# Kernel optimization log

Hardware: AMD Instinct MI355X
Metric: run time of the kernel (lower is better)

## Reference

```python
import jax, jax.numpy as jnp
import numpy as np
from jax import lax

EPS = 1e-08


def setup_inputs() -> dict:
    key = jax.random.key(0)
    k1, k2, k3 = jax.random.split(key, 3)
    b, cin, cout, ks, h, w = 16, 64, 64, 3, 256, 256
    X = jax.random.normal(k1, (b, cin, h, w), dtype=jnp.float32)
    y = jax.random.normal(k2, (b, cin), dtype=jnp.float32)
    weight = jax.random.normal(k3, (cout, cin, ks, ks), dtype=jnp.float32)
    return {"X": X, "y": y, "weight": weight}


def reference(X, y, weight):
    # EqualizedWeight: scale by Kaiming constant c = (cin*k*k)^-0.5 (gain=lr_mul=1)
    cout, cin, ks, _ = weight.shape
    c = (cin * ks * ks) ** (-0.5)
    w0 = weight * c
    # Modulate: per-sample, per-input-channel scaling -> (b, cout, cin, k, k)
    w1 = w0[None] * y[:, None, :, None, None]
    # Demodulate: normalize each (sample, out-filter) to unit L2 norm
    d = lax.rsqrt(jnp.sum(w1 * w1, axis=(2, 3, 4), keepdims=True) + EPS)
    w1 = w1 * d
    b, _, h, w = X.shape
    # Grouped conv: fold batch into channels, one group per sample
    Xr = X.reshape(1, b * cin, h, w)
    ker = w1.reshape(b * cout, cin, ks, ks)
    out = lax.conv_general_dilated(
        Xr, ker,
        window_strides=(1, 1),
        padding="SAME",
        feature_group_count=b,
        dimension_numbers=("NCHW", "OIHW", "NCHW"),
    )
    return out.reshape(b, cout, h, w)
```

## Files before the change

kernel.cpp:

```cpp
#include <hip/hip_runtime.h>
#include <hip/hip_bf16.h>

typedef __bf16 bf16x8 __attribute__((ext_vector_type(8)));
typedef float  f32x4  __attribute__((ext_vector_type(4)));

#define B_   16
#define CIN  64
#define COUT 64
#define H_   256
#define W_   256
#define TY   16
#define SLOT (258 * 64)

__global__ void modw_kernel(const float* __restrict__ weight,
                            const float* __restrict__ y,
                            __bf16* __restrict__ w1g) {
  const int co = blockIdx.x;
  const int b  = blockIdx.y;
  const int ci = threadIdx.x;
  const float c  = 0.041666666666666664f;
  const float yv = y[b*CIN + ci] * c;
  float w[9];
  float s = 0.0f;
#pragma unroll
  for (int t = 0; t < 9; ++t) {
    float wv = weight[(co*CIN + ci)*9 + t] * yv;
    w[t] = wv;
    s += wv * wv;
  }
#pragma unroll
  for (int off = 32; off > 0; off >>= 1) s += __shfl_xor(s, off, 64);
  const float d = rsqrtf(s + 1e-8f);
#pragma unroll
  for (int t = 0; t < 9; ++t)
    w1g[((b*9 + t)*COUT + co)*CIN + ci] = (__bf16)(w[t] * d);
}

__device__ __forceinline__ void stage_load(const float* __restrict__ X,
                                           int b, int yy, int tid, float4* f) {
  const int cg = tid >> 6;
  const int px_base = 4 * (tid & 63);
  const float* xrow = X + ((long)b * (CIN * H_ * W_) + (long)yy * W_);
#pragma unroll
  for (int j = 0; j < 8; ++j)
    f[j] = *reinterpret_cast<const float4*>(xrow + (long)(cg * 8 + j) * (H_ * W_) + px_base);
}

__device__ __forceinline__ void stage_write(__bf16* __restrict__ xs, int slot,
                                            int tid, const float4* f, bool valid) {
  const int cg = tid >> 6;
  const int px_base = 4 * (tid & 63);
  bf16x8 frag[4];
  if (valid) {
#pragma unroll
    for (int j = 0; j < 8; ++j) {
      frag[0][j] = (__bf16)f[j].x;
      frag[1][j] = (__bf16)f[j].y;
      frag[2][j] = (__bf16)f[j].z;
      frag[3][j] = (__bf16)f[j].w;
    }
  } else {
#pragma unroll
    for (int o = 0; o < 4; ++o)
#pragma unroll
      for (int j = 0; j < 8; ++j) frag[o][j] = (__bf16)0.f;
  }
#pragma unroll
  for (int oo = 0; oo < 4; ++oo) {
    const int o  = (oo + tid) & 3;
    const int pl = px_base + o + 1;
    const int gs = cg ^ (pl & 7);
    *reinterpret_cast<bf16x8*>(&xs[slot * SLOT + pl * 64 + gs * 8]) = frag[o];
  }
}

__global__ __launch_bounds__(512, 2)
void conv_kernel(const float* __restrict__ X,
                 const __bf16* __restrict__ w1g,
                 float* __restrict__ out) {
  const int y0   = blockIdx.x * TY;
  const int b    = blockIdx.y;
  const int tid  = threadIdx.x;
  const int lane = tid & 63;
  const int wv   = tid >> 6;
  const int cgw  = wv & 1;
  const int pg   = wv >> 1;
  const int q    = lane >> 4;
  const int n    = lane & 15;

  __shared__ __bf16 xs[3 * SLOT];

  if (tid < 384) {
    const int s = tid >> 7, r = tid & 127;
    const int col = (r < 64) ? 0 : 257;
    xs[s * SLOT + col * 64 + (r & 63)] = (__bf16)0.f;
  }

  bf16x8 wfr[2][9][2];
#pragma unroll
  for (int c2 = 0; c2 < 2; ++c2) {
    const int co = cgw * 32 + c2 * 16 + n;
#pragma unroll
    for (int tap = 0; tap < 9; ++tap) {
      const __bf16* wp = w1g + ((b * 9 + tap) * COUT + co) * CIN + q * 8;
      wfr[c2][tap][0] = *reinterpret_cast<const bf16x8*>(wp);
      wfr[c2][tap][1] = *reinterpret_cast<const bf16x8*>(wp + 32);
    }
  }

  {
    float4 f[8];
#pragma unroll
    for (int k = 0; k < 3; ++k) {
      const int yy = y0 - 1 + k;
      const bool valid = (yy >= 0);
      if (valid) stage_load(X, b, yy, tid, f);
      stage_write(xs, (yy + 3) % 3, tid, f, valid);
    }
  }

  float4 pf[8];
  for (int ty = 0; ty < TY; ++ty) {
    const int y = y0 + ty;
    __syncthreads();

    const int yy = y + 2;
    const bool do_pf = (ty < TY - 1);
    const bool pf_ok = do_pf && (yy < H_);
    if (pf_ok) stage_load(X, b, yy, tid, pf);

    f32x4 acc[2][4];
#pragma unroll
    for (int c2 = 0; c2 < 2; ++c2)
#pragma unroll
      for (int nt = 0; nt < 4; ++nt) acc[c2][nt] = (f32x4){0.f, 0.f, 0.f, 0.f};

#pragma unroll
    for (int dy = 0; dy < 3; ++dy) {
      const __bf16* sl = &xs[((y - 1 + dy + 3) % 3) * SLOT];
#pragma unroll
      for (int dx = 0; dx < 3; ++dx) {
        const int tap = dy * 3 + dx;
        const int p3 = (n + dx) & 7;
        const int o0 = (q ^ p3) * 8;
        const int o1 = ((q + 4) ^ p3) * 8;
#pragma unroll
        for (int nt = 0; nt < 4; ++nt) {
          const int px = pg * 64 + nt * 16 + n + dx;
          const bf16x8 a0 = *reinterpret_cast<const bf16x8*>(&sl[px * 64 + o0]);
          const bf16x8 a1 = *reinterpret_cast<const bf16x8*>(&sl[px * 64 + o1]);
          acc[0][nt] = __builtin_amdgcn_mfma_f32_16x16x32_bf16(a0, wfr[0][tap][0], acc[0][nt], 0, 0, 0);
          acc[0][nt] = __builtin_amdgcn_mfma_f32_16x16x32_bf16(a1, wfr[0][tap][1], acc[0][nt], 0, 0, 0);
          acc[1][nt] = __builtin_amdgcn_mfma_f32_16x16x32_bf16(a0, wfr[1][tap][0], acc[1][nt], 0, 0, 0);
          acc[1][nt] = __builtin_amdgcn_mfma_f32_16x16x32_bf16(a1, wfr[1][tap][1], acc[1][nt], 0, 0, 0);
        }
      }
    }
    __syncthreads();

#pragma unroll
    for (int c2 = 0; c2 < 2; ++c2) {
      const int co = cgw * 32 + c2 * 16 + n;
#pragma unroll
      for (int nt = 0; nt < 4; ++nt) {
        const int px0 = pg * 64 + nt * 16 + q * 4;
        *reinterpret_cast<float4*>(out + ((long)(b * COUT + co) * H_ + y) * W_ + px0) =
            *reinterpret_cast<const float4*>(&acc[c2][nt]);
      }
    }

    if (do_pf) stage_write(xs, yy % 3, tid, pf, pf_ok);
  }
}

extern "C" void kernel_launch(void* const* d_in, const int* in_sizes, int n_in,
                              void* d_out, int out_size, void* d_ws, size_t ws_size,
                              hipStream_t stream) {
  const float* X = (const float*)d_in[0];
  const float* y = (const float*)d_in[1];
  const float* w = (const float*)d_in[2];
  float* outp = (float*)d_out;
  __bf16* w1g = (__bf16*)d_ws;

  modw_kernel<<<dim3(COUT, B_), 64, 0, stream>>>(w, y, w1g);
  conv_kernel<<<dim3(H_ / TY, B_), 512, 0, stream>>>(X, w1g, outp);
}
```

Before: 606.1 us.

## Compute two output rows per iteration with a four-slot LDS row ring

The conv loop now produces two output rows per iteration from a four-row LDS ring instead of one row from a three-row ring. Each loaded input-row A-fragment feeds the MFMAs for both output rows. This cuts LDS reads per output row and halves the number of barriers and loop iterations. In exchange it doubles the accumulators and prefetch registers, which raises register pressure under the existing launch bounds and may cause spills. It also grows LDS use by one row slot.

```diff
diff --git a/kernel.cpp b/kernel.cpp
--- a/kernel.cpp
+++ b/kernel.cpp
@@ -88,9 +88,9 @@
   const int q    = lane >> 4;
   const int n    = lane & 15;
 
-  __shared__ __bf16 xs[3 * SLOT];
-
-  if (tid < 384) {
+  __shared__ __bf16 xs[4 * SLOT];
+
+  {
     const int s = tid >> 7, r = tid & 127;
     const int col = (r < 64) ? 0 : 257;
     xs[s * SLOT + col * 64 + (r & 63)] = (__bf16)0.f;
@@ -111,36 +111,39 @@
   {
     float4 f[8];
 #pragma unroll
-    for (int k = 0; k < 3; ++k) {
+    for (int k = 0; k < 4; ++k) {
       const int yy = y0 - 1 + k;
       const bool valid = (yy >= 0);
       if (valid) stage_load(X, b, yy, tid, f);
-      stage_write(xs, (yy + 3) % 3, tid, f, valid);
-    }
-  }
-
-  float4 pf[8];
-  for (int ty = 0; ty < TY; ++ty) {
-    const int y = y0 + ty;
+      stage_write(xs, (yy + 4) & 3, tid, f, valid);
+    }
+  }
+
+  float4 pfA[8], pfB[8];
+  for (int t2 = 0; t2 < TY / 2; ++t2) {
+    const int y = y0 + 2 * t2;
     __syncthreads();
 
-    const int yy = y + 2;
-    const bool do_pf = (ty < TY - 1);
-    const bool pf_ok = do_pf && (yy < H_);
-    if (pf_ok) stage_load(X, b, yy, tid, pf);
-
-    f32x4 acc[2][4];
-#pragma unroll
-    for (int c2 = 0; c2 < 2; ++c2)
-#pragma unroll
-      for (int nt = 0; nt < 4; ++nt) acc[c2][nt] = (f32x4){0.f, 0.f, 0.f, 0.f};
-
-#pragma unroll
-    for (int dy = 0; dy < 3; ++dy) {
-      const __bf16* sl = &xs[((y - 1 + dy + 3) % 3) * SLOT];
+    const bool do_pf = (t2 < TY / 2 - 1);
+    const int yA = y + 3, yB = y + 4;
+    const bool okA = do_pf && (yA < H_);
+    const bool okB = do_pf && (yB < H_);
+    if (okA) stage_load(X, b, yA, tid, pfA);
+    if (okB) stage_load(X, b, yB, tid, pfB);
+
+    f32x4 acc[2][2][4];
+#pragma unroll
+    for (int o = 0; o < 2; ++o)
+#pragma unroll
+      for (int c2 = 0; c2 < 2; ++c2)
+#pragma unroll
+        for (int nt = 0; nt < 4; ++nt) acc[o][c2][nt] = (f32x4){0.f, 0.f, 0.f, 0.f};
+
+#pragma unroll
+    for (int rr = 0; rr < 4; ++rr) {
+      const __bf16* sl = &xs[((y - 1 + rr + 4) & 3) * SLOT];
 #pragma unroll
       for (int dx = 0; dx < 3; ++dx) {
-        const int tap = dy * 3 + dx;
         const int p3 = (n + dx) & 7;
         const int o0 = (q ^ p3) * 8;
         const int o1 = ((q + 4) ^ p3) * 8;
@@ -149,27 +152,43 @@
           const int px = pg * 64 + nt * 16 + n + dx;
           const bf16x8 a0 = *reinterpret_cast<const bf16x8*>(&sl[px * 64 + o0]);
           const bf16x8 a1 = *reinterpret_cast<const bf16x8*>(&sl[px * 64 + o1]);
-          acc[0][nt] = __builtin_amdgcn_mfma_f32_16x16x32_bf16(a0, wfr[0][tap][0], acc[0][nt], 0, 0, 0);
-          acc[0][nt] = __builtin_amdgcn_mfma_f32_16x16x32_bf16(a1, wfr[0][tap][1], acc[0][nt], 0, 0, 0);
-          acc[1][nt] = __builtin_amdgcn_mfma_f32_16x16x32_bf16(a0, wfr[1][tap][0], acc[1][nt], 0, 0, 0);
-          acc[1][nt] = __builtin_amdgcn_mfma_f32_16x16x32_bf16(a1, wfr[1][tap][1], acc[1][nt], 0, 0, 0);
+          if (rr <= 2) {
+            const int tapA = rr * 3 + dx;
+            acc[0][0][nt] = __builtin_amdgcn_mfma_f32_16x16x32_bf16(a0, wfr[0][tapA][0], acc[0][0][nt], 0, 0, 0);
+            acc[0][0][nt] = __builtin_amdgcn_mfma_f32_16x16x32_bf16(a1, wfr[0][tapA][1], acc[0][0][nt], 0, 0, 0);
+            acc[0][1][nt] = __builtin_amdgcn_mfma_f32_16x16x32_bf16(a0, wfr[1][tapA][0], acc[0][1][nt], 0, 0, 0);
+            acc[0][1][nt] = __builtin_amdgcn_mfma_f32_16x16x32_bf16(a1, wfr[1][tapA][1], acc[0][1][nt], 0, 0, 0);
+          }
+          if (rr >= 1) {
+            const int tapB = (rr - 1) * 3 + dx;
+            acc[1][0][nt] = __builtin_amdgcn_mfma_f32_16x16x32_bf16(a0, wfr[0][tapB][0], acc[1][0][nt], 0, 0, 0);
+            acc[1][0][nt] = __builtin_amdgcn_mfma_f32_16x16x32_bf16(a1, wfr[0][tapB][1], acc[1][0][nt], 0, 0, 0);
+            acc[1][1][nt] = __builtin_amdgcn_mfma_f32_16x16x32_bf16(a0, wfr[1][tapB][0], acc[1][1][nt], 0, 0, 0);
+            acc[1][1][nt] = __builtin_amdgcn_mfma_f32_16x16x32_bf16(a1, wfr[1][tapB][1], acc[1][1][nt], 0, 0, 0);
+          }
         }
       }
     }
     __syncthreads();
 
 #pragma unroll
-    for (int c2 = 0; c2 < 2; ++c2) {
-      const int co = cgw * 32 + c2 * 16 + n;
-#pragma unroll
-      for (int nt = 0; nt < 4; ++nt) {
-        const int px0 = pg * 64 + nt * 16 + q * 4;
-        *reinterpret_cast<float4*>(out + ((long)(b * COUT + co) * H_ + y) * W_ + px0) =
-            *reinterpret_cast<const float4*>(&acc[c2][nt]);
+    for (int o = 0; o < 2; ++o) {
+#pragma unroll
+      for (int c2 = 0; c2 < 2; ++c2) {
+        const int co = cgw * 32 + c2 * 16 + n;
+#pragma unroll
+        for (int nt = 0; nt < 4; ++nt) {
+          const int px0 = pg * 64 + nt * 16 + q * 4;
+          *reinterpret_cast<float4*>(out + ((long)(b * COUT + co) * H_ + (y + o)) * W_ + px0) =
+              *reinterpret_cast<const float4*>(&acc[o][c2][nt]);
+        }
       }
     }
 
-    if (do_pf) stage_write(xs, yy % 3, tid, pf, pf_ok);
+    if (do_pf) {
+      stage_write(xs, (yA + 4) & 3, tid, pfA, okA);
+      stage_write(xs, (yB + 4) & 3, tid, pfB, okB);
+    }
   }
 }
 
```

New measurement: 835.1 us. 1.38x slower.

## Split conv tiles along width, reload weights per row, drop register prefetch

Applied to the files above, without the earlier changes.

The convolution now tiles along image width as well, using 128-pixel column tiles with 8-pixel halos and 256-thread blocks. This doubles the grid and shrinks the shared-memory row buffer so more blocks fit per CU. Weights are reloaded from global memory per kernel row instead of held in registers across all nine taps, which cuts register pressure. The register-based prefetch of the next row is replaced with a synchronous load-and-store after the output write, so that overlap is lost. It also adds MFMA priority hints, packs four output channels per block in the weight-modulation kernel, and adds scalar halo loads.

```diff
diff --git a/kernel.cpp b/kernel.cpp
--- a/kernel.cpp
+++ b/kernel.cpp
@@ -10,12 +10,14 @@
 #define H_   256
 #define W_   256
 #define TY   16
-#define SLOT (258 * 64)
+#define PXB  128
+#define SW   144
+#define SLOT3 (SW * 64)
 
 __global__ void modw_kernel(const float* __restrict__ weight,
                             const float* __restrict__ y,
                             __bf16* __restrict__ w1g) {
-  const int co = blockIdx.x;
+  const int co = blockIdx.x * 4 + threadIdx.y;
   const int b  = blockIdx.y;
   const int ci = threadIdx.x;
   const float c  = 0.041666666666666664f;
@@ -36,50 +38,60 @@
     w1g[((b*9 + t)*COUT + co)*CIN + ci] = (__bf16)(w[t] * d);
 }
 
-__device__ __forceinline__ void stage_load(const float* __restrict__ X,
-                                           int b, int yy, int tid, float4* f) {
-  const int cg = tid >> 6;
-  const int px_base = 4 * (tid & 63);
-  const float* xrow = X + ((long)b * (CIN * H_ * W_) + (long)yy * W_);
+__device__ __forceinline__ void stage_row(const float* __restrict__ X,
+                                          __bf16* __restrict__ xs, int slot,
+                                          int b, int yy, int x0, int tid) {
+  const bool rowok = (yy >= 0) && (yy < H_);
+  const float* xrow = X + ((long)b * (CIN * H_ * W_) + (long)(rowok ? yy : 0) * W_);
+  __bf16* sl = xs + slot * SLOT3;
+
+  {
+    const int cg   = tid >> 5;
+    const int pgid = tid & 31;
+    const int gpx  = x0 + 4 * pgid;
+    float4 f[8];
+    if (rowok) {
 #pragma unroll
-  for (int j = 0; j < 8; ++j)
-    f[j] = *reinterpret_cast<const float4*>(xrow + (long)(cg * 8 + j) * (H_ * W_) + px_base);
-}
-
-__device__ __forceinline__ void stage_write(__bf16* __restrict__ xs, int slot,
-                                            int tid, const float4* f, bool valid) {
-  const int cg = tid >> 6;
-  const int px_base = 4 * (tid & 63);
-  bf16x8 frag[4];
-  if (valid) {
-#pragma unroll
-    for (int j = 0; j < 8; ++j) {
-      frag[0][j] = (__bf16)f[j].x;
-      frag[1][j] = (__bf16)f[j].y;
-      frag[2][j] = (__bf16)f[j].z;
-      frag[3][j] = (__bf16)f[j].w;
+      for (int j = 0; j < 8; ++j)
+        f[j] = *reinterpret_cast<const float4*>(xrow + (long)(cg * 8 + j) * (H_ * W_) + gpx);
     }
-  } else {
+    bf16x8 frag[4];
 #pragma unroll
     for (int o = 0; o < 4; ++o)
 #pragma unroll
-      for (int j = 0; j < 8; ++j) frag[o][j] = (__bf16)0.f;
+      for (int j = 0; j < 8; ++j)
+        frag[o][j] = rowok ? (__bf16)((&f[j].x)[o]) : (__bf16)0.f;
+#pragma unroll
+    for (int oo = 0; oo < 4; ++oo) {
+      const int o  = (oo + tid) & 3;
+      const int pl = 8 + 4 * pgid + o;
+      const int gs = cg ^ (pl & 7);
+      *reinterpret_cast<bf16x8*>(&sl[pl * 64 + gs * 8]) = frag[o];
+    }
   }
+
+  if (tid < 128) {
+    const int i  = tid >> 3;
+    const int cg = tid & 7;
+    const int pl = (i < 8) ? i : (128 + i);
+    const int gpx = x0 - 8 + pl;
+    const bool ok = rowok && (gpx >= 0) && (gpx < W_);
+    bf16x8 v;
 #pragma unroll
-  for (int oo = 0; oo < 4; ++oo) {
-    const int o  = (oo + tid) & 3;
-    const int pl = px_base + o + 1;
+    for (int j = 0; j < 8; ++j)
+      v[j] = ok ? (__bf16)xrow[(long)(cg * 8 + j) * (H_ * W_) + gpx] : (__bf16)0.f;
     const int gs = cg ^ (pl & 7);
-    *reinterpret_cast<bf16x8*>(&xs[slot * SLOT + pl * 64 + gs * 8]) = frag[o];
+    *reinterpret_cast<bf16x8*>(&sl[pl * 64 + gs * 8]) = v;
   }
 }
 
-__global__ __launch_bounds__(512, 2)
+__global__ __launch_bounds__(256)
 void conv_kernel(const float* __restrict__ X,
                  const __bf16* __restrict__ w1g,
                  float* __restrict__ out) {
-  const int y0   = blockIdx.x * TY;
-  const int b    = blockIdx.y;
+  const int x0   = blockIdx.x * PXB;
+  const int y0   = blockIdx.y * TY;
+  const int b    = blockIdx.z;
   const int tid  = threadIdx.x;
   const int lane = tid & 63;
   const int wv   = tid >> 6;
@@ -88,46 +100,16 @@
   const int q    = lane >> 4;
   const int n    = lane & 15;
 
-  __shared__ __bf16 xs[3 * SLOT];
+  __shared__ __bf16 xs[3 * SLOT3];
 
-  if (tid < 384) {
-    const int s = tid >> 7, r = tid & 127;
-    const int col = (r < 64) ? 0 : 257;
-    xs[s * SLOT + col * 64 + (r & 63)] = (__bf16)0.f;
+  for (int k = 0; k < 3; ++k) {
+    const int yy = y0 - 1 + k;
+    stage_row(X, xs, (yy + 1) % 3, b, yy, x0, tid);
   }
 
-  bf16x8 wfr[2][9][2];
-#pragma unroll
-  for (int c2 = 0; c2 < 2; ++c2) {
-    const int co = cgw * 32 + c2 * 16 + n;
-#pragma unroll
-    for (int tap = 0; tap < 9; ++tap) {
-      const __bf16* wp = w1g + ((b * 9 + tap) * COUT + co) * CIN + q * 8;
-      wfr[c2][tap][0] = *reinterpret_cast<const bf16x8*>(wp);
-      wfr[c2][tap][1] = *reinterpret_cast<const bf16x8*>(wp + 32);
-    }
-  }
-
-  {
-    float4 f[8];
-#pragma unroll
-    for (int k = 0; k < 3; ++k) {
-      const int yy = y0 - 1 + k;
-      const bool valid = (yy >= 0);
-      if (valid) stage_load(X, b, yy, tid, f);
-      stage_write(xs, (yy + 3) % 3, tid, f, valid);
-    }
-  }
-
-  float4 pf[8];
   for (int ty = 0; ty < TY; ++ty) {
     const int y = y0 + ty;
     __syncthreads();
-
-    const int yy = y + 2;
-    const bool do_pf = (ty < TY - 1);
-    const bool pf_ok = do_pf && (yy < H_);
-    if (pf_ok) stage_load(X, b, yy, tid, pf);
 
     f32x4 acc[2][4];
 #pragma unroll
@@ -135,27 +117,41 @@
 #pragma unroll
       for (int nt = 0; nt < 4; ++nt) acc[c2][nt] = (f32x4){0.f, 0.f, 0.f, 0.f};
 
+    __builtin_amdgcn_s_setprio(1);
 #pragma unroll
     for (int dy = 0; dy < 3; ++dy) {
-      const __bf16* sl = &xs[((y - 1 + dy + 3) % 3) * SLOT];
+      const __bf16* sl = &xs[((y + dy) % 3) * SLOT3];
+
+      bf16x8 wfr[2][3][2];
+#pragma unroll
+      for (int c2 = 0; c2 < 2; ++c2) {
+        const int co = cgw * 32 + c2 * 16 + n;
+#pragma unroll
+        for (int dx = 0; dx < 3; ++dx) {
+          const __bf16* wp = w1g + ((b * 9 + dy * 3 + dx) * COUT + co) * CIN + q * 8;
+          wfr[c2][dx][0] = *reinterpret_cast<const bf16x8*>(wp);
+          wfr[c2][dx][1] = *reinterpret_cast<const bf16x8*>(wp + 32);
+        }
+      }
+
 #pragma unroll
       for (int dx = 0; dx < 3; ++dx) {
-        const int tap = dy * 3 + dx;
-        const int p3 = (n + dx) & 7;
+        const int p3 = (n + dx + 7) & 7;
         const int o0 = (q ^ p3) * 8;
         const int o1 = ((q + 4) ^ p3) * 8;
 #pragma unroll
         for (int nt = 0; nt < 4; ++nt) {
-          const int px = pg * 64 + nt * 16 + n + dx;
-          const bf16x8 a0 = *reinterpret_cast<const bf16x8*>(&sl[px * 64 + o0]);
-          const bf16x8 a1 = *reinterpret_cast<const bf16x8*>(&sl[px * 64 + o1]);
-          acc[0][nt] = __builtin_amdgcn_mfma_f32_16x16x32_bf16(a0, wfr[0][tap][0], acc[0][nt], 0, 0, 0);
-          acc[0][nt] = __builtin_amdgcn_mfma_f32_16x16x32_bf16(a1, wfr[0][tap][1], acc[0][nt], 0, 0, 0);
-          acc[1][nt] = __builtin_amdgcn_mfma_f32_16x16x32_bf16(a0, wfr[1][tap][0], acc[1][nt], 0, 0, 0);
-          acc[1][nt] = __builtin_amdgcn_mfma_f32_16x16x32_bf16(a1, wfr[1][tap][1], acc[1][nt], 0, 0, 0);
+          const int pl = pg * 64 + nt * 16 + n + dx + 7;
+          const bf16x8 a0 = *reinterpret_cast<const bf16x8*>(&sl[pl * 64 + o0]);
+          const bf16x8 a1 = *reinterpret_cast<const bf16x8*>(&sl[pl * 64 + o1]);
+          acc[0][nt] = __builtin_amdgcn_mfma_f32_16x16x32_bf16(a0, wfr[0][dx][0], acc[0][nt], 0, 0, 0);
+          acc[0][nt] = __builtin_amdgcn_mfma_f32_16x16x32_bf16(a1, wfr[0][dx][1], acc[0][nt], 0, 0, 0);
+          acc[1][nt] = __builtin_amdgcn_mfma_f32_16x16x32_bf16(a0, wfr[1][dx][0], acc[1][nt], 0, 0, 0);
+          acc[1][nt] = __builtin_amdgcn_mfma_f32_16x16x32_bf16(a1, wfr[1][dx][1], acc[1][nt], 0, 0, 0);
         }
       }
     }
+    __builtin_amdgcn_s_setprio(0);
     __syncthreads();
 
 #pragma unroll
@@ -163,13 +159,14 @@
       const int co = cgw * 32 + c2 * 16 + n;
 #pragma unroll
       for (int nt = 0; nt < 4; ++nt) {
-        const int px0 = pg * 64 + nt * 16 + q * 4;
+        const int px0 = x0 + pg * 64 + nt * 16 + q * 4;
         *reinterpret_cast<float4*>(out + ((long)(b * COUT + co) * H_ + y) * W_ + px0) =
             *reinterpret_cast<const float4*>(&acc[c2][nt]);
       }
     }
 
-    if (do_pf) stage_write(xs, yy % 3, tid, pf, pf_ok);
+    if (ty < TY - 1)
+      stage_row(X, xs, (y + 3) % 3, b, y + 2, x0, tid);
   }
 }
 
@@ -182,6 +179,6 @@
   float* outp = (float*)d_out;
   __bf16* w1g = (__bf16*)d_ws;
 
-  modw_kernel<<<dim3(COUT, B_), 64, 0, stream>>>(w, y, w1g);
-  conv_kernel<<<dim3(H_ / TY, B_), 512, 0, stream>>>(X, w1g, outp);
+  modw_kernel<<<dim3(COUT / 4, B_), dim3(64, 4), 0, stream>>>(w, y, w1g);
+  conv_kernel<<<dim3(W_ / PXB, H_ / TY, B_), 256, 0, stream>>>(X, w1g, outp);
 }
```

New measurement: 812.5 us. 34.1% more time.
